# Performance work log

Measured on AMD Instinct MI355X. Metric: run time of the kernel, lower is better.

Reference implementation:

```python
import jax, jax.numpy as jnp
import numpy as np

N_QUBITS = 6
N_LAYERS = 2
FEATURE_DIMS = [768, 512, 1024]
BATCH = 16384
PI = np.float32(np.pi)
C64 = jnp.complex64


def _ry(t):
    c = jnp.cos(t / 2).astype(C64)
    s = jnp.sin(t / 2).astype(C64)
    return jnp.stack([jnp.stack([c, -s], -1), jnp.stack([s, c], -1)], -2)


def _rx(t):
    c = jnp.cos(t / 2).astype(C64)
    s = (-1j * jnp.sin(t / 2).astype(C64))
    return jnp.stack([jnp.stack([c, s], -1), jnp.stack([s, c], -1)], -2)


def _rz(t):
    e = jnp.exp(-0.5j * t.astype(C64))
    z = jnp.zeros_like(e)
    return jnp.stack([jnp.stack([e, z], -1), jnp.stack([z, jnp.conj(e)], -1)], -2)


def _apply_1q(state, gate, wire):
    # state: [B, 2,...,2]; gate: [2,2] (shared) or [B,2,2] (per-sample)
    s = jnp.moveaxis(state, wire + 1, -1)
    shp = s.shape
    s = s.reshape(shp[0], -1, 2)
    if gate.ndim == 2:
        s = jnp.einsum('ij,bkj->bki', gate, s)
    else:
        s = jnp.einsum('bij,bkj->bki', gate, s)
    return jnp.moveaxis(s.reshape(shp), -1, wire + 1)


def _apply_cnot(state, control, target):
    s = jnp.moveaxis(state, (control + 1, target + 1), (1, 2))
    s = jnp.stack([s[:, 0], s[:, 1, ::-1]], axis=1)
    return jnp.moveaxis(s, (1, 2), (control + 1, target + 1))


def _apply_cry(state, theta, control, target):
    s = jnp.moveaxis(state, (control + 1, target + 1), (1, 2))
    g = _ry(theta)  # [2,2]
    c1 = jnp.einsum('ij,bj...->bi...', g, s[:, 1])
    s = jnp.stack([s[:, 0], c1], axis=1)
    return jnp.moveaxis(s, (1, 2), (control + 1, target + 1))


def run_circuit(angles, qw):
    # angles: [B, n_qubits] encoding RY angles; qw: [n_layers, n_qubits, 3]
    B = angles.shape[0]
    n = N_QUBITS
    state = jnp.zeros((B,) + (2,) * n, C64).at[(slice(None),) + (0,) * n].set(1.0)
    # encoding: sequential RYs on a wire compose to RY(sum of angles); RY(0) is identity
    for i in range(n):
        state = _apply_1q(state, _ry(angles[:, i]), i)
    for l in range(N_LAYERS):
        for i in range(n):
            state = _apply_1q(state, _rx(qw[l, i, 0]), i)
            state = _apply_1q(state, _ry(qw[l, i, 1]), i)
            state = _apply_1q(state, _rz(qw[l, i, 2]), i)
        for i in range(n - 1):
            state = _apply_cnot(state, i, i + 1)
        if n > 2:
            state = _apply_cnot(state, 0, n - 1)
        for i in range(0, n - 1, 2):
            state = _apply_cry(state, qw[l, i, 1], i, i + 1)
    probs = state.real ** 2 + state.imag ** 2  # [B, 2,...,2]
    z = [(jnp.take(probs, 0, axis=i + 1) - jnp.take(probs, 1, axis=i + 1)).reshape(B, -1).sum(-1)
         for i in range(n)]
    return jnp.stack(z, axis=-1)  # [B, n_qubits]


def setup_inputs() -> dict:
    key = jax.random.key(0)
    ks = jax.random.split(key, 10)
    inp = {}
    for m, d in enumerate(FEATURE_DIMS):
        inp[f'feat{m}'] = jax.random.normal(ks[m], (BATCH, d), jnp.float32)
        inp[f'W{m}'] = jax.random.normal(ks[3 + m], (d, N_QUBITS), jnp.float32) / np.sqrt(d)
        inp[f'b{m}'] = jnp.zeros((N_QUBITS,), jnp.float32)
    inp['qw'] = 0.1 * jax.random.normal(ks[6], (N_LAYERS, N_QUBITS, 3), jnp.float32)
    inp['fusion_logits'] = jnp.ones((len(FEATURE_DIMS),), jnp.float32) / len(FEATURE_DIMS)
    return inp


def reference(feat0, feat1, feat2, W0, b0, W1, b1, W2, b2, qw, fusion_logits):
    fw = jax.nn.softmax(fusion_logits)
    q0 = jnp.tanh(feat0 @ W0 + b0)  # [B, n_qubits]
    q1 = jnp.tanh(feat1 @ W1 + b1)
    q2 = jnp.tanh(feat2 @ W2 + b2)
    angles = PI * (fw[0] * q0 + fw[1] * q1 + fw[2] * q2)
    return run_circuit(angles, qw)
```

## Files before the change

### kernel.cpp

```cpp
#include <hip/hip_runtime.h>

#define PI_F 3.14159265358979323846f

#define D0 768
#define D1 512
#define D2 1024
#define WT_FLOATS 13824
#define U_OFF   WT_FLOATS
#define CRY_OFF (WT_FLOATS + 48)


__global__ void prep_kernel(const float* __restrict__ W0, const float* __restrict__ W1,
                            const float* __restrict__ W2, const float* __restrict__ qw,
                            float* __restrict__ ws) {
    int t = blockIdx.x * 256 + threadIdx.x;
    if (t < 4608) {
        int j = t / 768, k = t - j * 768;
        ws[t] = W0[k * 6 + j];
    } else if (t < 7680) {
        int u = t - 4608, j = u / 512, k = u - j * 512;
        ws[t] = W1[k * 6 + j];
    } else if (t < WT_FLOATS) {
        int u = t - 7680, j = u / 1024, k = u - j * 1024;
        ws[t] = W2[k * 6 + j];
    } else if (t < WT_FLOATS + 12) {
        int g = t - WT_FLOATS;
        float ca, sa, cb, sb, cc, sc;
        sincosf(0.5f * qw[g * 3 + 0], &sa, &ca);
        sincosf(0.5f * qw[g * 3 + 1], &sb, &cb);
        sincosf(0.5f * qw[g * 3 + 2], &sc, &cc);
        float m00r = cb * ca, m00i = sb * sa;
        float m01r = -sb * ca, m01i = -cb * sa;
        float* u4 = ws + U_OFF + g * 4;
        u4[0] = m00r * cc + m00i * sc;
        u4[1] = m00i * cc - m00r * sc;
        u4[2] = m01r * cc + m01i * sc;
        u4[3] = m01i * cc - m01r * sc;
    } else if (t < WT_FLOATS + 18) {
        int k = t - WT_FLOATS - 12;
        int l = k / 3, i = (k - l * 3) * 2;
        float c, s;
        sincosf(0.5f * qw[(l * 6 + i) * 3 + 1], &s, &c);
        ws[CRY_OFF + k * 2 + 0] = c;
        ws[CRY_OFF + k * 2 + 1] = s;
    }
}


template<int CTRL>
__device__ __forceinline__ float dppmov(float v) {
    return __int_as_float(__builtin_amdgcn_update_dpp(0, __float_as_int(v), CTRL, 0xF, 0xF, true));
}
template<int PAT>
__device__ __forceinline__ float swzf(float v) {
    return __int_as_float(__builtin_amdgcn_ds_swizzle(__float_as_int(v), PAT));
}

template<int M>
__device__ __forceinline__ float xsh(float v) {
    if constexpr (M == 1)       return dppmov<0xB1>(v);
    else if constexpr (M == 2)  return dppmov<0x4E>(v);
    else if constexpr (M == 4)  return swzf<0x101F>(v);
    else if constexpr (M == 8)  return dppmov<0x128>(v);
    else if constexpr (M == 16) return swzf<0x401F>(v);
    else                        return __shfl_xor(v, 32, 64);
}

__device__ __forceinline__ float pl16_sum(float v) {
#if __has_builtin(__builtin_amdgcn_permlane16_swap)
    auto r = __builtin_amdgcn_permlane16_swap(__float_as_uint(v), __float_as_uint(v), false, false);
    return __uint_as_float(r[0]) + __uint_as_float(r[1]);
#else
    return v + swzf<0x401F>(v);
#endif
}
__device__ __forceinline__ float pl32_sum(float v) {
#if __has_builtin(__builtin_amdgcn_permlane32_swap)
    auto r = __builtin_amdgcn_permlane32_swap(__float_as_uint(v), __float_as_uint(v), false, false);
    return __uint_as_float(r[0]) + __uint_as_float(r[1]);
#else
    return v + __shfl_xor(v, 32, 64);
#endif
}

__device__ __forceinline__ float fast_tanh(float x) {
    float e = __expf(2.0f * x);
    return 1.0f - 2.0f / (e + 1.0f);
}

__device__ __forceinline__ float dot4(float4 a, float4 w, float acc) {
    return fmaf(a.x, w.x, fmaf(a.y, w.y, fmaf(a.z, w.z, fmaf(a.w, w.w, acc))));
}


template<int M>
__device__ __forceinline__ void gateU(float (&re)[2], float (&im)[2], int lane,
                                      float ar, float ai, float br, float bi) {
    const bool hi = (lane & M) != 0;
    const float Ai = hi ? -ai : ai;
    const float Br = hi ? -br : br;
#pragma unroll
    for (int s = 0; s < 2; ++s) {
        float pre = xsh<M>(re[s]);
        float pim = xsh<M>(im[s]);
        float nr = ar * re[s] - Ai * im[s] + Br * pre - bi * pim;
        float ni = ar * im[s] + Ai * re[s] + Br * pim + bi * pre;
        re[s] = nr; im[s] = ni;
    }
}

template<int MC, int MT>
__device__ __forceinline__ void gateCRY(float (&re)[2], float (&im)[2], int lane, float c, float sn) {
    const bool c1 = (lane & MC) != 0;
    const float sg = (lane & MT) ? sn : -sn;
#pragma unroll
    for (int s = 0; s < 2; ++s) {
        float pre = xsh<MT>(re[s]);
        float pim = xsh<MT>(im[s]);
        float nr = fmaf(c, re[s], sg * pre);
        float ni = fmaf(c, im[s], sg * pim);
        re[s] = c1 ? nr : re[s];
        im[s] = c1 ? ni : im[s];
    }
}

template<int I>
__device__ __forceinline__ void l1gate(float (&re)[2], float (&im)[2], int lane,
                                       const float* __restrict__ ws) {
    constexpr int M = 32 >> I;
    const float ar = ws[U_OFF + (6 + I) * 4 + 0];
    const float ai = ws[U_OFF + (6 + I) * 4 + 1];
    const float br = ws[U_OFF + (6 + I) * 4 + 2];
    const float bi = ws[U_OFF + (6 + I) * 4 + 3];
    gateU<M>(re, im, lane, ar, ai, br, bi);
}

template<int L, int P>
__device__ __forceinline__ void cryGate(float (&re)[2], float (&im)[2], int lane,
                                        const float* __restrict__ ws) {
    constexpr int MC = 32 >> (2 * P);
    constexpr int MT = 16 >> (2 * P);
    const float c = ws[CRY_OFF + (L * 3 + P) * 2 + 0];
    const float s = ws[CRY_OFF + (L * 3 + P) * 2 + 1];
    gateCRY<MC, MT>(re, im, lane, c, s);
}

__device__ __forceinline__ void buildState(const float (&ang)[6], int lane,
                                           const float* __restrict__ ws,
                                           float& reO, float& imO) {
    float pr, pi;
#pragma unroll
    for (int i = 0; i < 6; ++i) {
        float cq, sq;
        __sincosf(0.5f * ang[i], &sq, &cq);
        const float ar = ws[U_OFF + i * 4 + 0];
        const float ai = ws[U_OFF + i * 4 + 1];
        const float br = ws[U_OFF + i * 4 + 2];
        const float bi = ws[U_OFF + i * 4 + 3];
        float vloR = ar * cq + br * sq;
        float vloI = ai * cq + bi * sq;
        float vhiR = ar * sq - br * cq;
        float vhiI = bi * cq - ai * sq;
        bool hi = (lane & (32 >> i)) != 0;
        float vr = hi ? vhiR : vloR;
        float vi = hi ? vhiI : vloI;
        if (i == 0) { pr = vr; pi = vi; }
        else { float t = pr * vr - pi * vi; pi = pr * vi + pi * vr; pr = t; }
    }
    reO = pr; imO = pi;
}


__global__ __launch_bounds__(256, 4) void qf_main(
    const float* __restrict__ f0, const float* __restrict__ b0,
    const float* __restrict__ f1, const float* __restrict__ b1,
    const float* __restrict__ f2, const float* __restrict__ b2,
    const float* __restrict__ fl, const float* __restrict__ ws,
    float* __restrict__ out)
{
    const int lane = threadIdx.x & 63;
    const int wave = blockIdx.x * 4 + (threadIdx.x >> 6);
    const int s0 = wave * 2;

    const float4* __restrict__ xA0 = (const float4*)(f0 + (size_t)s0 * D0);
    const float4* __restrict__ xB0 = (const float4*)(f0 + (size_t)(s0 + 1) * D0);
    const float4* __restrict__ xA1 = (const float4*)(f1 + (size_t)s0 * D1);
    const float4* __restrict__ xB1 = (const float4*)(f1 + (size_t)(s0 + 1) * D1);
    const float4* __restrict__ xA2 = (const float4*)(f2 + (size_t)s0 * D2);
    const float4* __restrict__ xB2 = (const float4*)(f2 + (size_t)(s0 + 1) * D2);

    float4 xa0 = xA0[lane], xa1 = xA0[64 + lane], xa2 = xA0[128 + lane];
    float4 xb0 = xB0[lane], xb1 = xB0[64 + lane], xb2 = xB0[128 + lane];
    float4 xa3 = xA1[lane], xa4 = xA1[64 + lane];
    float4 xb3 = xB1[lane], xb4 = xB1[64 + lane];
    __builtin_amdgcn_sched_barrier(0);

    float l0 = fl[0], l1 = fl[1], l2 = fl[2];
    float mx = fmaxf(l0, fmaxf(l1, l2));
    float e0 = __expf(l0 - mx), e1 = __expf(l1 - mx), e2 = __expf(l2 - mx);
    float inv = 1.0f / (e0 + e1 + e2);
    float fw0 = e0 * inv, fw1 = e1 * inv, fw2 = e2 * inv;

    const float4* __restrict__ w4 = (const float4*)ws;
    float r[36];

#pragma unroll
    for (int j = 0; j < 6; ++j) {
        float4 w0 = w4[j * 192 + lane];
        float4 w1 = w4[j * 192 + 64 + lane];
        float4 w2 = w4[j * 192 + 128 + lane];
        float a = 0.f, b = 0.f;
        a = dot4(xa0, w0, a); a = dot4(xa1, w1, a); a = dot4(xa2, w2, a);
        b = dot4(xb0, w0, b); b = dot4(xb1, w1, b); b = dot4(xb2, w2, b);
        r[j] = a; r[6 + j] = b;
    }

    float4 xa5 = xA2[lane], xa6 = xA2[64 + lane], xa7 = xA2[128 + lane], xa8 = xA2[192 + lane];
    float4 xb5 = xB2[lane], xb6 = xB2[64 + lane], xb7 = xB2[128 + lane], xb8 = xB2[192 + lane];
    __builtin_amdgcn_sched_barrier(0);

#pragma unroll
    for (int j = 0; j < 6; ++j) {
        float4 w0 = w4[1152 + j * 128 + lane];
        float4 w1 = w4[1152 + j * 128 + 64 + lane];
        float a = 0.f, b = 0.f;
        a = dot4(xa3, w0, a); a = dot4(xa4, w1, a);
        b = dot4(xb3, w0, b); b = dot4(xb4, w1, b);
        r[12 + j] = a; r[18 + j] = b;
    }

#pragma unroll
    for (int j = 0; j < 6; ++j) {
        float4 w0 = w4[1920 + j * 256 + lane];
        float4 w1 = w4[1920 + j * 256 + 64 + lane];
        float4 w2 = w4[1920 + j * 256 + 128 + lane];
        float4 w3 = w4[1920 + j * 256 + 192 + lane];
        float a = 0.f, b = 0.f;
        a = dot4(xa5, w0, a); a = dot4(xa6, w1, a); a = dot4(xa7, w2, a); a = dot4(xa8, w3, a);
        b = dot4(xb5, w0, b); b = dot4(xb6, w1, b); b = dot4(xb7, w2, b); b = dot4(xb8, w3, b);
        r[24 + j] = a; r[30 + j] = b;
    }

#pragma unroll
    for (int k = 0; k < 36; ++k) r[k] += dppmov<0xB1>(r[k]);
#pragma unroll
    for (int k = 0; k < 36; ++k) r[k] += dppmov<0x4E>(r[k]);
#pragma unroll
    for (int k = 0; k < 36; ++k) r[k] += swzf<0x101F>(r[k]);
#pragma unroll
    for (int k = 0; k < 36; ++k) r[k] += dppmov<0x128>(r[k]);
#pragma unroll
    for (int k = 0; k < 36; ++k) r[k] = pl16_sum(r[k]);
#pragma unroll
    for (int k = 0; k < 36; ++k) r[k] = pl32_sum(r[k]);

    float angA[6], angB[6];
#pragma unroll
    for (int j = 0; j < 6; ++j) {
        float tA0 = fast_tanh(r[j]      + b0[j]);
        float tB0 = fast_tanh(r[6 + j]  + b0[j]);
        float tA1 = fast_tanh(r[12 + j] + b1[j]);
        float tB1 = fast_tanh(r[18 + j] + b1[j]);
        float tA2 = fast_tanh(r[24 + j] + b2[j]);
        float tB2 = fast_tanh(r[30 + j] + b2[j]);
        angA[j] = PI_F * (fw0 * tA0 + fw1 * tA1 + fw2 * tA2);
        angB[j] = PI_F * (fw0 * tB0 + fw1 * tB1 + fw2 * tB2);
    }

    const int sigma = lane ^ ((lane >> 1) & 0x1F) ^ ((lane >> 5) & 1);

    float re[2], im[2];
    buildState(angA, lane, ws, re[0], im[0]);
    buildState(angB, lane, ws, re[1], im[1]);

    re[0] = __shfl(re[0], sigma, 64); im[0] = __shfl(im[0], sigma, 64);
    re[1] = __shfl(re[1], sigma, 64); im[1] = __shfl(im[1], sigma, 64);
    cryGate<0,0>(re, im, lane, ws); cryGate<0,1>(re, im, lane, ws); cryGate<0,2>(re, im, lane, ws);

    l1gate<0>(re, im, lane, ws); l1gate<1>(re, im, lane, ws); l1gate<2>(re, im, lane, ws);
    l1gate<3>(re, im, lane, ws); l1gate<4>(re, im, lane, ws); l1gate<5>(re, im, lane, ws);
    re[0] = __shfl(re[0], sigma, 64); im[0] = __shfl(im[0], sigma, 64);
    re[1] = __shfl(re[1], sigma, 64); im[1] = __shfl(im[1], sigma, 64);
    cryGate<1,0>(re, im, lane, ws); cryGate<1,1>(re, im, lane, ws); cryGate<1,2>(re, im, lane, ws);

#pragma unroll
    for (int s = 0; s < 2; ++s) {
        float p = fmaf(re[s], re[s], im[s] * im[s]);
        float q;
        q = xsh<1>(p);  p = (lane & 1)  ? (q - p) : (p + q);
        q = xsh<2>(p);  p = (lane & 2)  ? (q - p) : (p + q);
        q = xsh<4>(p);  p = (lane & 4)  ? (q - p) : (p + q);
        q = xsh<8>(p);  p = (lane & 8)  ? (q - p) : (p + q);
        q = xsh<16>(p); p = (lane & 16) ? (q - p) : (p + q);
        q = xsh<32>(p); p = (lane & 32) ? (q - p) : (p + q);
        if (__popc(lane) == 1)
            out[(size_t)(s0 + s) * 6 + (6 - __ffs(lane))] = p;
    }
}

extern "C" void kernel_launch(void* const* d_in, const int* in_sizes, int n_in,
                              void* d_out, int out_size, void* d_ws, size_t ws_size,
                              hipStream_t stream) {
    const float* f0 = (const float*)d_in[0];
    const float* W0 = (const float*)d_in[1];
    const float* b0 = (const float*)d_in[2];
    const float* f1 = (const float*)d_in[3];
    const float* W1 = (const float*)d_in[4];
    const float* b1 = (const float*)d_in[5];
    const float* f2 = (const float*)d_in[6];
    const float* W2 = (const float*)d_in[7];
    const float* b2 = (const float*)d_in[8];
    const float* qw = (const float*)d_in[9];
    const float* fl = (const float*)d_in[10];
    float* out = (float*)d_out;
    float* ws = (float*)d_ws;

    prep_kernel<<<55, 256, 0, stream>>>(W0, W1, W2, qw, ws);
    qf_main<<<2048, 256, 0, stream>>>(f0, b0, f1, b1, f2, b2, fl, ws, out);
}
```

Measured before the change: 46.39 us.

## Stage transposed weights in LDS and process two sample pairs per wave

```diff
diff --git a/kernel.cpp b/kernel.cpp
--- a/kernel.cpp
+++ b/kernel.cpp
@@ -55,7 +55,6 @@
 __device__ __forceinline__ float swzf(float v) {
     return __int_as_float(__builtin_amdgcn_ds_swizzle(__float_as_int(v), PAT));
 }
-
 template<int M>
 __device__ __forceinline__ float xsh(float v) {
     if constexpr (M == 1)       return dppmov<0xB1>(v);
@@ -65,7 +64,6 @@
     else if constexpr (M == 16) return swzf<0x401F>(v);
     else                        return __shfl_xor(v, 32, 64);
 }
-
 __device__ __forceinline__ float pl16_sum(float v) {
 #if __has_builtin(__builtin_amdgcn_permlane16_swap)
     auto r = __builtin_amdgcn_permlane16_swap(__float_as_uint(v), __float_as_uint(v), false, false);
@@ -82,12 +80,10 @@
     return v + __shfl_xor(v, 32, 64);
 #endif
 }
-
 __device__ __forceinline__ float fast_tanh(float x) {
     float e = __expf(2.0f * x);
     return 1.0f - 2.0f / (e + 1.0f);
 }
-
 __device__ __forceinline__ float dot4(float4 a, float4 w, float acc) {
     return fmaf(a.x, w.x, fmaf(a.y, w.y, fmaf(a.z, w.z, fmaf(a.w, w.w, acc))));
 }
@@ -108,7 +104,6 @@
         re[s] = nr; im[s] = ni;
     }
 }
-
 template<int MC, int MT>
 __device__ __forceinline__ void gateCRY(float (&re)[2], float (&im)[2], int lane, float c, float sn) {
     const bool c1 = (lane & MC) != 0;
@@ -123,28 +118,21 @@
         im[s] = c1 ? ni : im[s];
     }
 }
-
 template<int I>
 __device__ __forceinline__ void l1gate(float (&re)[2], float (&im)[2], int lane,
                                        const float* __restrict__ ws) {
     constexpr int M = 32 >> I;
-    const float ar = ws[U_OFF + (6 + I) * 4 + 0];
-    const float ai = ws[U_OFF + (6 + I) * 4 + 1];
-    const float br = ws[U_OFF + (6 + I) * 4 + 2];
-    const float bi = ws[U_OFF + (6 + I) * 4 + 3];
-    gateU<M>(re, im, lane, ar, ai, br, bi);
-}
-
+    gateU<M>(re, im, lane, ws[U_OFF + (6 + I) * 4 + 0], ws[U_OFF + (6 + I) * 4 + 1],
+             ws[U_OFF + (6 + I) * 4 + 2], ws[U_OFF + (6 + I) * 4 + 3]);
+}
 template<int L, int P>
 __device__ __forceinline__ void cryGate(float (&re)[2], float (&im)[2], int lane,
                                         const float* __restrict__ ws) {
     constexpr int MC = 32 >> (2 * P);
     constexpr int MT = 16 >> (2 * P);
-    const float c = ws[CRY_OFF + (L * 3 + P) * 2 + 0];
-    const float s = ws[CRY_OFF + (L * 3 + P) * 2 + 1];
-    gateCRY<MC, MT>(re, im, lane, c, s);
-}
-
+    gateCRY<MC, MT>(re, im, lane, ws[CRY_OFF + (L * 3 + P) * 2 + 0],
+                    ws[CRY_OFF + (L * 3 + P) * 2 + 1]);
+}
 __device__ __forceinline__ void buildState(const float (&ang)[6], int lane,
                                            const float* __restrict__ ws,
                                            float& reO, float& imO) {
@@ -171,29 +159,19 @@
 }
 
 
-__global__ __launch_bounds__(256, 4) void qf_main(
+__global__ __launch_bounds__(512, 4) void qf_main(
     const float* __restrict__ f0, const float* __restrict__ b0,
     const float* __restrict__ f1, const float* __restrict__ b1,
     const float* __restrict__ f2, const float* __restrict__ b2,
     const float* __restrict__ fl, const float* __restrict__ ws,
     float* __restrict__ out)
 {
+    __shared__ __align__(16) float sW[WT_FLOATS];
+    for (int i = threadIdx.x; i < WT_FLOATS; i += 512) sW[i] = ws[i];
+    __syncthreads();
+
     const int lane = threadIdx.x & 63;
-    const int wave = blockIdx.x * 4 + (threadIdx.x >> 6);
-    const int s0 = wave * 2;
-
-    const float4* __restrict__ xA0 = (const float4*)(f0 + (size_t)s0 * D0);
-    const float4* __restrict__ xB0 = (const float4*)(f0 + (size_t)(s0 + 1) * D0);
-    const float4* __restrict__ xA1 = (const float4*)(f1 + (size_t)s0 * D1);
-    const float4* __restrict__ xB1 = (const float4*)(f1 + (size_t)(s0 + 1) * D1);
-    const float4* __restrict__ xA2 = (const float4*)(f2 + (size_t)s0 * D2);
-    const float4* __restrict__ xB2 = (const float4*)(f2 + (size_t)(s0 + 1) * D2);
-
-    float4 xa0 = xA0[lane], xa1 = xA0[64 + lane], xa2 = xA0[128 + lane];
-    float4 xb0 = xB0[lane], xb1 = xB0[64 + lane], xb2 = xB0[128 + lane];
-    float4 xa3 = xA1[lane], xa4 = xA1[64 + lane];
-    float4 xb3 = xB1[lane], xb4 = xB1[64 + lane];
-    __builtin_amdgcn_sched_barrier(0);
+    const int wv = blockIdx.x * 8 + (threadIdx.x >> 6);
 
     float l0 = fl[0], l1 = fl[1], l2 = fl[2];
     float mx = fmaxf(l0, fmaxf(l1, l2));
@@ -201,100 +179,113 @@
     float inv = 1.0f / (e0 + e1 + e2);
     float fw0 = e0 * inv, fw1 = e1 * inv, fw2 = e2 * inv;
 
-    const float4* __restrict__ w4 = (const float4*)ws;
-    float r[36];
-
-#pragma unroll
-    for (int j = 0; j < 6; ++j) {
-        float4 w0 = w4[j * 192 + lane];
-        float4 w1 = w4[j * 192 + 64 + lane];
-        float4 w2 = w4[j * 192 + 128 + lane];
-        float a = 0.f, b = 0.f;
-        a = dot4(xa0, w0, a); a = dot4(xa1, w1, a); a = dot4(xa2, w2, a);
-        b = dot4(xb0, w0, b); b = dot4(xb1, w1, b); b = dot4(xb2, w2, b);
-        r[j] = a; r[6 + j] = b;
-    }
-
-    float4 xa5 = xA2[lane], xa6 = xA2[64 + lane], xa7 = xA2[128 + lane], xa8 = xA2[192 + lane];
-    float4 xb5 = xB2[lane], xb6 = xB2[64 + lane], xb7 = xB2[128 + lane], xb8 = xB2[192 + lane];
-    __builtin_amdgcn_sched_barrier(0);
-
-#pragma unroll
-    for (int j = 0; j < 6; ++j) {
-        float4 w0 = w4[1152 + j * 128 + lane];
-        float4 w1 = w4[1152 + j * 128 + 64 + lane];
-        float a = 0.f, b = 0.f;
-        a = dot4(xa3, w0, a); a = dot4(xa4, w1, a);
-        b = dot4(xb3, w0, b); b = dot4(xb4, w1, b);
-        r[12 + j] = a; r[18 + j] = b;
-    }
-
-#pragma unroll
-    for (int j = 0; j < 6; ++j) {
-        float4 w0 = w4[1920 + j * 256 + lane];
-        float4 w1 = w4[1920 + j * 256 + 64 + lane];
-        float4 w2 = w4[1920 + j * 256 + 128 + lane];
-        float4 w3 = w4[1920 + j * 256 + 192 + lane];
-        float a = 0.f, b = 0.f;
-        a = dot4(xa5, w0, a); a = dot4(xa6, w1, a); a = dot4(xa7, w2, a); a = dot4(xa8, w3, a);
-        b = dot4(xb5, w0, b); b = dot4(xb6, w1, b); b = dot4(xb7, w2, b); b = dot4(xb8, w3, b);
-        r[24 + j] = a; r[30 + j] = b;
-    }
-
-#pragma unroll
-    for (int k = 0; k < 36; ++k) r[k] += dppmov<0xB1>(r[k]);
-#pragma unroll
-    for (int k = 0; k < 36; ++k) r[k] += dppmov<0x4E>(r[k]);
-#pragma unroll
-    for (int k = 0; k < 36; ++k) r[k] += swzf<0x101F>(r[k]);
-#pragma unroll
-    for (int k = 0; k < 36; ++k) r[k] += dppmov<0x128>(r[k]);
-#pragma unroll
-    for (int k = 0; k < 36; ++k) r[k] = pl16_sum(r[k]);
-#pragma unroll
-    for (int k = 0; k < 36; ++k) r[k] = pl32_sum(r[k]);
-
-    float angA[6], angB[6];
-#pragma unroll
-    for (int j = 0; j < 6; ++j) {
-        float tA0 = fast_tanh(r[j]      + b0[j]);
-        float tB0 = fast_tanh(r[6 + j]  + b0[j]);
-        float tA1 = fast_tanh(r[12 + j] + b1[j]);
-        float tB1 = fast_tanh(r[18 + j] + b1[j]);
-        float tA2 = fast_tanh(r[24 + j] + b2[j]);
-        float tB2 = fast_tanh(r[30 + j] + b2[j]);
-        angA[j] = PI_F * (fw0 * tA0 + fw1 * tA1 + fw2 * tA2);
-        angB[j] = PI_F * (fw0 * tB0 + fw1 * tB1 + fw2 * tB2);
-    }
-
     const int sigma = lane ^ ((lane >> 1) & 0x1F) ^ ((lane >> 5) & 1);
 
-    float re[2], im[2];
-    buildState(angA, lane, ws, re[0], im[0]);
-    buildState(angB, lane, ws, re[1], im[1]);
-
-    re[0] = __shfl(re[0], sigma, 64); im[0] = __shfl(im[0], sigma, 64);
-    re[1] = __shfl(re[1], sigma, 64); im[1] = __shfl(im[1], sigma, 64);
-    cryGate<0,0>(re, im, lane, ws); cryGate<0,1>(re, im, lane, ws); cryGate<0,2>(re, im, lane, ws);
-
-    l1gate<0>(re, im, lane, ws); l1gate<1>(re, im, lane, ws); l1gate<2>(re, im, lane, ws);
-    l1gate<3>(re, im, lane, ws); l1gate<4>(re, im, lane, ws); l1gate<5>(re, im, lane, ws);
-    re[0] = __shfl(re[0], sigma, 64); im[0] = __shfl(im[0], sigma, 64);
-    re[1] = __shfl(re[1], sigma, 64); im[1] = __shfl(im[1], sigma, 64);
-    cryGate<1,0>(re, im, lane, ws); cryGate<1,1>(re, im, lane, ws); cryGate<1,2>(re, im, lane, ws);
-
-#pragma unroll
-    for (int s = 0; s < 2; ++s) {
-        float p = fmaf(re[s], re[s], im[s] * im[s]);
-        float q;
-        q = xsh<1>(p);  p = (lane & 1)  ? (q - p) : (p + q);
-        q = xsh<2>(p);  p = (lane & 2)  ? (q - p) : (p + q);
-        q = xsh<4>(p);  p = (lane & 4)  ? (q - p) : (p + q);
-        q = xsh<8>(p);  p = (lane & 8)  ? (q - p) : (p + q);
-        q = xsh<16>(p); p = (lane & 16) ? (q - p) : (p + q);
-        q = xsh<32>(p); p = (lane & 32) ? (q - p) : (p + q);
-        if (__popc(lane) == 1)
-            out[(size_t)(s0 + s) * 6 + (6 - __ffs(lane))] = p;
+    for (int bt = 0; bt < 2; ++bt) {
+        const int s0 = wv * 4 + bt * 2;
+
+        const float* pA0 = f0 + (size_t)s0 * D0 + lane * 4;
+        const float* pB0 = pA0 + D0;
+        const float* pA1 = f1 + (size_t)s0 * D1 + lane * 4;
+        const float* pB1 = pA1 + D1;
+        const float* pA2 = f2 + (size_t)s0 * D2 + lane * 4;
+        const float* pB2 = pA2 + D2;
+        float4 xa[9], xb[9];
+        xa[0] = *(const float4*)(pA0);        xa[1] = *(const float4*)(pA0 + 256);
+        xa[2] = *(const float4*)(pA0 + 512);
+        xb[0] = *(const float4*)(pB0);        xb[1] = *(const float4*)(pB0 + 256);
+        xb[2] = *(const float4*)(pB0 + 512);
+        xa[3] = *(const float4*)(pA1);        xa[4] = *(const float4*)(pA1 + 256);
+        xb[3] = *(const float4*)(pB1);        xb[4] = *(const float4*)(pB1 + 256);
+        xa[5] = *(const float4*)(pA2);        xa[6] = *(const float4*)(pA2 + 256);
+        xa[7] = *(const float4*)(pA2 + 512);  xa[8] = *(const float4*)(pA2 + 768);
+        xb[5] = *(const float4*)(pB2);        xb[6] = *(const float4*)(pB2 + 256);
+        xb[7] = *(const float4*)(pB2 + 512);  xb[8] = *(const float4*)(pB2 + 768);
+
+        float r[36];
+#pragma unroll
+        for (int k = 0; k < 36; ++k) r[k] = 0.f;
+#pragma unroll
+        for (int it = 0; it < 3; ++it) {
+#pragma unroll
+            for (int j = 0; j < 6; ++j) {
+                float4 w = *(const float4*)&sW[j * 768 + it * 256 + lane * 4];
+                r[j]     = dot4(xa[it], w, r[j]);
+                r[6 + j] = dot4(xb[it], w, r[6 + j]);
+            }
+        }
+#pragma unroll
+        for (int it = 0; it < 2; ++it) {
+#pragma unroll
+            for (int j = 0; j < 6; ++j) {
+                float4 w = *(const float4*)&sW[4608 + j * 512 + it * 256 + lane * 4];
+                r[12 + j] = dot4(xa[3 + it], w, r[12 + j]);
+                r[18 + j] = dot4(xb[3 + it], w, r[18 + j]);
+            }
+        }
+#pragma unroll
+        for (int it = 0; it < 4; ++it) {
+#pragma unroll
+            for (int j = 0; j < 6; ++j) {
+                float4 w = *(const float4*)&sW[7680 + j * 1024 + it * 256 + lane * 4];
+                r[24 + j] = dot4(xa[5 + it], w, r[24 + j]);
+                r[30 + j] = dot4(xb[5 + it], w, r[30 + j]);
+            }
+        }
+
+#pragma unroll
+        for (int k = 0; k < 36; ++k) r[k] += dppmov<0xB1>(r[k]);
+#pragma unroll
+        for (int k = 0; k < 36; ++k) r[k] += dppmov<0x4E>(r[k]);
+#pragma unroll
+        for (int k = 0; k < 36; ++k) r[k] += swzf<0x101F>(r[k]);
+#pragma unroll
+        for (int k = 0; k < 36; ++k) r[k] += dppmov<0x128>(r[k]);
+#pragma unroll
+        for (int k = 0; k < 36; ++k) r[k] = pl16_sum(r[k]);
+#pragma unroll
+        for (int k = 0; k < 36; ++k) r[k] = pl32_sum(r[k]);
+
+        float angA[6], angB[6];
+#pragma unroll
+        for (int j = 0; j < 6; ++j) {
+            float tA0 = fast_tanh(r[j]      + b0[j]);
+            float tB0 = fast_tanh(r[6 + j]  + b0[j]);
+            float tA1 = fast_tanh(r[12 + j] + b1[j]);
+            float tB1 = fast_tanh(r[18 + j] + b1[j]);
+            float tA2 = fast_tanh(r[24 + j] + b2[j]);
+            float tB2 = fast_tanh(r[30 + j] + b2[j]);
+            angA[j] = PI_F * (fw0 * tA0 + fw1 * tA1 + fw2 * tA2);
+            angB[j] = PI_F * (fw0 * tB0 + fw1 * tB1 + fw2 * tB2);
+        }
+
+        float re[2], im[2];
+        buildState(angA, lane, ws, re[0], im[0]);
+        buildState(angB, lane, ws, re[1], im[1]);
+
+        re[0] = __shfl(re[0], sigma, 64); im[0] = __shfl(im[0], sigma, 64);
+        re[1] = __shfl(re[1], sigma, 64); im[1] = __shfl(im[1], sigma, 64);
+        cryGate<0,0>(re, im, lane, ws); cryGate<0,1>(re, im, lane, ws); cryGate<0,2>(re, im, lane, ws);
+
+        l1gate<0>(re, im, lane, ws); l1gate<1>(re, im, lane, ws); l1gate<2>(re, im, lane, ws);
+        l1gate<3>(re, im, lane, ws); l1gate<4>(re, im, lane, ws); l1gate<5>(re, im, lane, ws);
+        re[0] = __shfl(re[0], sigma, 64); im[0] = __shfl(im[0], sigma, 64);
+        re[1] = __shfl(re[1], sigma, 64); im[1] = __shfl(im[1], sigma, 64);
+        cryGate<1,0>(re, im, lane, ws); cryGate<1,1>(re, im, lane, ws); cryGate<1,2>(re, im, lane, ws);
+
+#pragma unroll
+        for (int s = 0; s < 2; ++s) {
+            float p = fmaf(re[s], re[s], im[s] * im[s]);
+            float q;
+            q = xsh<1>(p);  p = (lane & 1)  ? (q - p) : (p + q);
+            q = xsh<2>(p);  p = (lane & 2)  ? (q - p) : (p + q);
+            q = xsh<4>(p);  p = (lane & 4)  ? (q - p) : (p + q);
+            q = xsh<8>(p);  p = (lane & 8)  ? (q - p) : (p + q);
+            q = xsh<16>(p); p = (lane & 16) ? (q - p) : (p + q);
+            q = xsh<32>(p); p = (lane & 32) ? (q - p) : (p + q);
+            if (__popc(lane) == 1)
+                out[(size_t)(s0 + s) * 6 + (6 - __ffs(lane))] = p;
+        }
     }
 }
 
@@ -316,5 +307,5 @@
     float* ws = (float*)d_ws;
 
     prep_kernel<<<55, 256, 0, stream>>>(W0, W1, W2, qw, ws);
-    qf_main<<<2048, 256, 0, stream>>>(f0, b0, f1, b1, f2, b2, fl, ws, out);
-}
+    qf_main<<<512, 512, 0, stream>>>(f0, b0, f1, b1, f2, b2, fl, ws, out);
+}
```

After: 168.3 us. 3.63x slower.
